# Kernel optimization log

Hardware: AMD Instinct MI355X
Metric: run time of the kernel (lower is better)

Reference implementation:

```python
import jax, jax.numpy as jnp
from jax import lax
import numpy as np

H = 256   # hidden size (hard-coded in module)
V = 10    # output classes


def setup_inputs() -> dict:
    key = jax.random.key(0)
    ks = jax.random.split(key, 7)
    B, T = 2048, 256
    x = jax.random.normal(ks[0], (B, T, 1), dtype=jnp.float32)
    # Linear weights stored as (in, out); torch nn.Linear computes x @ W.T + b,
    # equivalent here to x @ W_inout + b.
    s1 = 1.0  # fan_in of embed is 1
    sH = 1.0 / np.sqrt(H)
    W_e = jax.random.uniform(ks[1], (1, H), jnp.float32, -s1, s1)
    b_e = jax.random.uniform(ks[2], (H,), jnp.float32, -s1, s1)
    W_h = jax.random.uniform(ks[3], (H, H), jnp.float32, -sH, sH)
    b_h = jax.random.uniform(ks[4], (H,), jnp.float32, -sH, sH)
    W_o = jax.random.uniform(ks[5], (H, V), jnp.float32, -sH, sH)
    b_o = jax.random.uniform(ks[6], (V,), jnp.float32, -sH, sH)
    return {"x": x, "W_e": W_e, "b_e": b_e, "W_h": W_h, "b_h": b_h,
            "W_o": W_o, "b_o": b_o}


def reference(x, W_e, b_e, W_h, b_h, W_o, b_o):
    B, T, _ = x.shape
    # Embedding of each timestep is independent of h -> precompute in one batched op.
    inp_all = jnp.tanh(x @ W_e + b_e)            # [B, T, H]
    inp_tbh = jnp.swapaxes(inp_all, 0, 1)        # [T, B, H] for scan

    def step(h, inp_t):
        h = jnp.tanh((inp_t + h) @ W_h + b_h)    # [B, H]
        return h, None

    h0 = jnp.zeros((B, H), dtype=x.dtype)
    h_final, _ = lax.scan(step, h0, inp_tbh)
    return h_final @ W_o + b_o                   # [B, V]
```

## Files before the change

kernel.cpp:

```cpp
#include <hip/hip_runtime.h>

#define HDIM 256
#define TDIM 256
#define VOUT 10
#define BC   8

typedef _Float16 f16x8 __attribute__((ext_vector_type(8)));
typedef float    f32x4 __attribute__((ext_vector_type(4)));

__device__ __forceinline__ float fast_tanh(float a) {
    float e = __expf(2.0f * a);
    return 1.0f - 2.0f * __builtin_amdgcn_rcpf(e + 1.0f);
}

__device__ __forceinline__ unsigned pkrtz_u32(float a, float b) {
    auto v = __builtin_amdgcn_cvt_pkrtz(a, b);
    union { decltype(v) h; unsigned u; } cvt;
    cvt.h = v;
    return cvt.u;
}

__global__ __launch_bounds__(512, 1) void rnn_fwd_v13(
    const float* __restrict__ x,
    const float* __restrict__ We,
    const float* __restrict__ be,
    const float* __restrict__ Wh,
    const float* __restrict__ bh,
    const float* __restrict__ Wo,
    const float* __restrict__ bo,
    float* __restrict__ out)
{
    __shared__ __align__(16) char vraw[2][BC * HDIM * 2];
    __shared__ float x_lds[BC][TDIM + 2];
    __shared__ float h_fin[BC][HDIM + 1];

    const int tid = threadIdx.x;
    const int l   = tid & 63;
    const int w   = tid >> 6;
    const int n   = l & 15;
    const int rn  = n & 7;
    const int hi  = n >> 3;
    const int g   = l >> 4;
    const int r0  = blockIdx.x * BC;

    for (int k = tid; k < BC * TDIM; k += 512) {
        int r = k >> 8, t = k & 255;
        x_lds[r][t] = x[(r0 + r) * TDIM + t];
    }

    f16x8 wfrag[2][8];
    #pragma unroll
    for (int mt = 0; mt < 2; ++mt) {
        const int col = 32 * w + 16 * mt + n;
        #pragma unroll
        for (int kt = 0; kt < 8; ++kt) {
            #pragma unroll
            for (int e = 0; e < 8; ++e)
                wfrag[mt][kt][e] = (_Float16)Wh[(kt * 32 + g * 8 + e) * HDIM + col];
        }
    }

    f32x4 bh0, bh1;
    #pragma unroll
    for (int rg = 0; rg < 4; ++rg) {
        bh0[rg] = bh[32 * w + 4 * g + rg];
        bh1[rg] = bh[32 * w + 16 + 4 * g + rg];
    }

    float WeO[2][2], beO[2][2];
    #pragma unroll
    for (int mt = 0; mt < 2; ++mt) {
        const int hc = 32 * w + 16 * mt + 4 * g + 2 * hi;
        WeO[mt][0] = We[hc];     beO[mt][0] = be[hc];
        WeO[mt][1] = We[hc + 1]; beO[mt][1] = be[hc + 1];
    }

    const int base_r = g * 128 + rn * 16;
    int addr_w[2];
    #pragma unroll
    for (int mt = 0; mt < 2; ++mt)
        addr_w[mt] = (4 * w + 2 * mt + (g >> 1)) * 128 + rn * 16 + (g & 1) * 8 + hi * 4;

    __syncthreads();

    {
        const float xv = x_lds[rn][0];
        #pragma unroll
        for (int mt = 0; mt < 2; ++mt) {
            const float s0 = fast_tanh(xv * WeO[mt][0] + beO[mt][0]);
            const float s1 = fast_tanh(xv * WeO[mt][1] + beO[mt][1]);
            *(unsigned*)(&vraw[0][0] + addr_w[mt]) = pkrtz_u32(s0, s1);
        }
    }
    __syncthreads();

    int cur = 0;
    #pragma unroll 1
    for (int t = 0; t < TDIM - 1; ++t) {
        const char* vr = &vraw[cur][0];
        char*       vw = &vraw[cur ^ 1][0];

        const float xv = x_lds[rn][t + 1];
        f16x8 bfrag[8];
        #pragma unroll
        for (int kt = 0; kt < 8; ++kt)
            bfrag[kt] = *(const f16x8*)(vr + base_r + kt * 512);

        const f32x4 zero = {0.f, 0.f, 0.f, 0.f};
        f32x4 accE0 = __builtin_amdgcn_mfma_f32_16x16x32_f16(wfrag[0][0], bfrag[0], bh0,  0, 0, 0);
        f32x4 accE1 = __builtin_amdgcn_mfma_f32_16x16x32_f16(wfrag[1][0], bfrag[0], bh1,  0, 0, 0);
        f32x4 accO0 = __builtin_amdgcn_mfma_f32_16x16x32_f16(wfrag[0][1], bfrag[1], zero, 0, 0, 0);
        f32x4 accO1 = __builtin_amdgcn_mfma_f32_16x16x32_f16(wfrag[1][1], bfrag[1], zero, 0, 0, 0);
        #pragma unroll
        for (int kp = 1; kp < 4; ++kp) {
            accE0 = __builtin_amdgcn_mfma_f32_16x16x32_f16(wfrag[0][2 * kp],     bfrag[2 * kp],     accE0, 0, 0, 0);
            accE1 = __builtin_amdgcn_mfma_f32_16x16x32_f16(wfrag[1][2 * kp],     bfrag[2 * kp],     accE1, 0, 0, 0);
            accO0 = __builtin_amdgcn_mfma_f32_16x16x32_f16(wfrag[0][2 * kp + 1], bfrag[2 * kp + 1], accO0, 0, 0, 0);
            accO1 = __builtin_amdgcn_mfma_f32_16x16x32_f16(wfrag[1][2 * kp + 1], bfrag[2 * kp + 1], accO1, 0, 0, 0);
        }

        __builtin_amdgcn_sched_barrier(0);

        float ipp[2][2];
        #pragma unroll
        for (int mt = 0; mt < 2; ++mt) {
            ipp[mt][0] = 1.0f + fast_tanh(xv * WeO[mt][0] + beO[mt][0]);
            ipp[mt][1] = 1.0f + fast_tanh(xv * WeO[mt][1] + beO[mt][1]);
        }

        {
            const float a0 = (hi ? accE0[2] : accE0[0]) + (hi ? accO0[2] : accO0[0]);
            const float a1 = (hi ? accE0[3] : accE0[1]) + (hi ? accO0[3] : accO0[1]);
            const float r0v = __builtin_amdgcn_rcpf(__expf(2.0f * a0) + 1.0f);
            const float r1v = __builtin_amdgcn_rcpf(__expf(2.0f * a1) + 1.0f);
            const float s0 = fmaf(-2.0f, r0v, ipp[0][0]);
            const float s1 = fmaf(-2.0f, r1v, ipp[0][1]);
            *(unsigned*)(vw + addr_w[0]) = pkrtz_u32(s0, s1);
        }
        {
            const float a0 = (hi ? accE1[2] : accE1[0]) + (hi ? accO1[2] : accO1[0]);
            const float a1 = (hi ? accE1[3] : accE1[1]) + (hi ? accO1[3] : accO1[1]);
            const float r0v = __builtin_amdgcn_rcpf(__expf(2.0f * a0) + 1.0f);
            const float r1v = __builtin_amdgcn_rcpf(__expf(2.0f * a1) + 1.0f);
            const float s0 = fmaf(-2.0f, r0v, ipp[1][0]);
            const float s1 = fmaf(-2.0f, r1v, ipp[1][1]);
            *(unsigned*)(vw + addr_w[1]) = pkrtz_u32(s0, s1);
        }
        cur ^= 1;
        __syncthreads();
    }

    {
        const char* vr = &vraw[cur][0];
        f16x8 bfrag[8];
        #pragma unroll
        for (int kt = 0; kt < 8; ++kt)
            bfrag[kt] = *(const f16x8*)(vr + base_r + kt * 512);

        const f32x4 zero = {0.f, 0.f, 0.f, 0.f};
        f32x4 accE0 = __builtin_amdgcn_mfma_f32_16x16x32_f16(wfrag[0][0], bfrag[0], bh0,  0, 0, 0);
        f32x4 accE1 = __builtin_amdgcn_mfma_f32_16x16x32_f16(wfrag[1][0], bfrag[0], bh1,  0, 0, 0);
        f32x4 accO0 = __builtin_amdgcn_mfma_f32_16x16x32_f16(wfrag[0][1], bfrag[1], zero, 0, 0, 0);
        f32x4 accO1 = __builtin_amdgcn_mfma_f32_16x16x32_f16(wfrag[1][1], bfrag[1], zero, 0, 0, 0);
        #pragma unroll
        for (int kp = 1; kp < 4; ++kp) {
            accE0 = __builtin_amdgcn_mfma_f32_16x16x32_f16(wfrag[0][2 * kp],     bfrag[2 * kp],     accE0, 0, 0, 0);
            accE1 = __builtin_amdgcn_mfma_f32_16x16x32_f16(wfrag[1][2 * kp],     bfrag[2 * kp],     accE1, 0, 0, 0);
            accO0 = __builtin_amdgcn_mfma_f32_16x16x32_f16(wfrag[0][2 * kp + 1], bfrag[2 * kp + 1], accO0, 0, 0, 0);
            accO1 = __builtin_amdgcn_mfma_f32_16x16x32_f16(wfrag[1][2 * kp + 1], bfrag[2 * kp + 1], accO1, 0, 0, 0);
        }
        {
            const float a0 = (hi ? accE0[2] : accE0[0]) + (hi ? accO0[2] : accO0[0]);
            const float a1 = (hi ? accE0[3] : accE0[1]) + (hi ? accO0[3] : accO0[1]);
            const int hc = 32 * w + 4 * g + 2 * hi;
            h_fin[rn][hc + 0] = fast_tanh(a0);
            h_fin[rn][hc + 1] = fast_tanh(a1);
        }
        {
            const float a0 = (hi ? accE1[2] : accE1[0]) + (hi ? accO1[2] : accO1[0]);
            const float a1 = (hi ? accE1[3] : accE1[1]) + (hi ? accO1[3] : accO1[1]);
            const int hc = 32 * w + 16 + 4 * g + 2 * hi;
            h_fin[rn][hc + 0] = fast_tanh(a0);
            h_fin[rn][hc + 1] = fast_tanh(a1);
        }
    }
    __syncthreads();

    if (tid < BC * VOUT) {
        const int r = tid / VOUT, vc = tid - r * VOUT;
        float sacc = bo[vc];
        #pragma unroll 8
        for (int i = 0; i < HDIM; ++i)
            sacc = fmaf(h_fin[r][i], Wo[i * VOUT + vc], sacc);
        out[(r0 + r) * VOUT + vc] = sacc;
    }
}

extern "C" void kernel_launch(void* const* d_in, const int* in_sizes, int n_in,
                              void* d_out, int out_size, void* d_ws, size_t ws_size,
                              hipStream_t stream) {
    const float* x  = (const float*)d_in[0];
    const float* We = (const float*)d_in[1];
    const float* be = (const float*)d_in[2];
    const float* Wh = (const float*)d_in[3];
    const float* bh = (const float*)d_in[4];
    const float* Wo = (const float*)d_in[5];
    const float* bo = (const float*)d_in[6];
    float* out = (float*)d_out;

    const int B = in_sizes[0] / TDIM;
    const int nblocks = B / BC;

    rnn_fwd_v13<<<nblocks, 512, 0, stream>>>(x, We, be, Wh, bh, Wo, bo, out);
}
```

Before: 161.1 us.

## Prescale weights by two, remap lane output columns, hoist input tanh before MFMAs

New measurement: 149.9 us. -6.9%, faster.

```diff
diff --git a/kernel.cpp b/kernel.cpp
--- a/kernel.cpp
+++ b/kernel.cpp
@@ -8,8 +8,8 @@
 typedef _Float16 f16x8 __attribute__((ext_vector_type(8)));
 typedef float    f32x4 __attribute__((ext_vector_type(4)));
 
-__device__ __forceinline__ float fast_tanh(float a) {
-    float e = __expf(2.0f * a);
+__device__ __forceinline__ float tanh_2a(float u) {
+    float e = __expf(u);
     return 1.0f - 2.0f * __builtin_amdgcn_rcpf(e + 1.0f);
 }
 
@@ -20,7 +20,7 @@
     return cvt.u;
 }
 
-__global__ __launch_bounds__(512, 1) void rnn_fwd_v13(
+__global__ __launch_bounds__(512, 1) void rnn_fwd_v16(
     const float* __restrict__ x,
     const float* __restrict__ We,
     const float* __restrict__ be,
@@ -56,46 +56,45 @@
         for (int kt = 0; kt < 8; ++kt) {
             #pragma unroll
             for (int e = 0; e < 8; ++e)
-                wfrag[mt][kt][e] = (_Float16)Wh[(kt * 32 + g * 8 + e) * HDIM + col];
+                wfrag[mt][kt][e] = (_Float16)(2.0f * Wh[(kt * 32 + g * 8 + e) * HDIM + col]);
         }
     }
 
     f32x4 bh0, bh1;
     #pragma unroll
     for (int rg = 0; rg < 4; ++rg) {
-        bh0[rg] = bh[32 * w + 4 * g + rg];
-        bh1[rg] = bh[32 * w + 16 + 4 * g + rg];
-    }
-
-    float WeO[2][2], beO[2][2];
+        bh0[rg] = 2.0f * bh[32 * w + 4 * g + rg];
+        bh1[rg] = 2.0f * bh[32 * w + 16 + 4 * g + rg];
+    }
+
+    const int hc0 = 32 * w + 16 * hi + 4 * g;
+    float WeX[4], beX[4];
     #pragma unroll
-    for (int mt = 0; mt < 2; ++mt) {
-        const int hc = 32 * w + 16 * mt + 4 * g + 2 * hi;
-        WeO[mt][0] = We[hc];     beO[mt][0] = be[hc];
-        WeO[mt][1] = We[hc + 1]; beO[mt][1] = be[hc + 1];
+    for (int j = 0; j < 4; ++j) {
+        WeX[j] = 2.0f * We[hc0 + j];
+        beX[j] = 2.0f * be[hc0 + j];
     }
 
     const int base_r = g * 128 + rn * 16;
-    int addr_w[2];
-    #pragma unroll
-    for (int mt = 0; mt < 2; ++mt)
-        addr_w[mt] = (4 * w + 2 * mt + (g >> 1)) * 128 + rn * 16 + (g & 1) * 8 + hi * 4;
+    const int addr_w = (4 * w + 2 * hi + (g >> 1)) * 128 + rn * 16 + (g & 1) * 8;
 
     __syncthreads();
 
     {
         const float xv = x_lds[rn][0];
-        #pragma unroll
-        for (int mt = 0; mt < 2; ++mt) {
-            const float s0 = fast_tanh(xv * WeO[mt][0] + beO[mt][0]);
-            const float s1 = fast_tanh(xv * WeO[mt][1] + beO[mt][1]);
-            *(unsigned*)(&vraw[0][0] + addr_w[mt]) = pkrtz_u32(s0, s1);
-        }
+        float s[4];
+        #pragma unroll
+        for (int j = 0; j < 4; ++j)
+            s[j] = tanh_2a(fmaf(xv, WeX[j], beX[j]));
+        uint2 pk;
+        pk.x = pkrtz_u32(s[0], s[1]);
+        pk.y = pkrtz_u32(s[2], s[3]);
+        *(uint2*)(&vraw[0][0] + addr_w) = pk;
     }
     __syncthreads();
 
     int cur = 0;
-    #pragma unroll 1
+    #pragma unroll 2
     for (int t = 0; t < TDIM - 1; ++t) {
         const char* vr = &vraw[cur][0];
         char*       vw = &vraw[cur ^ 1][0];
@@ -105,6 +104,15 @@
         #pragma unroll
         for (int kt = 0; kt < 8; ++kt)
             bfrag[kt] = *(const f16x8*)(vr + base_r + kt * 512);
+
+        float ipp[4];
+        #pragma unroll
+        for (int j = 0; j < 4; ++j) {
+            const float u = fmaf(xv, WeX[j], beX[j]);
+            const float e = __expf(u);
+            const float r = __builtin_amdgcn_rcpf(e + 1.0f);
+            ipp[j] = fmaf(-2.0f, r, 2.0f);
+        }
 
         const f32x4 zero = {0.f, 0.f, 0.f, 0.f};
         f32x4 accE0 = __builtin_amdgcn_mfma_f32_16x16x32_f16(wfrag[0][0], bfrag[0], bh0,  0, 0, 0);
@@ -119,32 +127,19 @@
             accO1 = __builtin_amdgcn_mfma_f32_16x16x32_f16(wfrag[1][2 * kp + 1], bfrag[2 * kp + 1], accO1, 0, 0, 0);
         }
 
-        __builtin_amdgcn_sched_barrier(0);
-
-        float ipp[2][2];
-        #pragma unroll
-        for (int mt = 0; mt < 2; ++mt) {
-            ipp[mt][0] = 1.0f + fast_tanh(xv * WeO[mt][0] + beO[mt][0]);
-            ipp[mt][1] = 1.0f + fast_tanh(xv * WeO[mt][1] + beO[mt][1]);
-        }
-
         {
-            const float a0 = (hi ? accE0[2] : accE0[0]) + (hi ? accO0[2] : accO0[0]);
-            const float a1 = (hi ? accE0[3] : accE0[1]) + (hi ? accO0[3] : accO0[1]);
-            const float r0v = __builtin_amdgcn_rcpf(__expf(2.0f * a0) + 1.0f);
-            const float r1v = __builtin_amdgcn_rcpf(__expf(2.0f * a1) + 1.0f);
-            const float s0 = fmaf(-2.0f, r0v, ipp[0][0]);
-            const float s1 = fmaf(-2.0f, r1v, ipp[0][1]);
-            *(unsigned*)(vw + addr_w[0]) = pkrtz_u32(s0, s1);
-        }
-        {
-            const float a0 = (hi ? accE1[2] : accE1[0]) + (hi ? accO1[2] : accO1[0]);
-            const float a1 = (hi ? accE1[3] : accE1[1]) + (hi ? accO1[3] : accO1[1]);
-            const float r0v = __builtin_amdgcn_rcpf(__expf(2.0f * a0) + 1.0f);
-            const float r1v = __builtin_amdgcn_rcpf(__expf(2.0f * a1) + 1.0f);
-            const float s0 = fmaf(-2.0f, r0v, ipp[1][0]);
-            const float s1 = fmaf(-2.0f, r1v, ipp[1][1]);
-            *(unsigned*)(vw + addr_w[1]) = pkrtz_u32(s0, s1);
+            float sj[4];
+            #pragma unroll
+            for (int j = 0; j < 4; ++j) {
+                const float a = (hi ? accE1[j] : accE0[j]) + (hi ? accO1[j] : accO0[j]);
+                const float e = __expf(a);
+                const float r = __builtin_amdgcn_rcpf(e + 1.0f);
+                sj[j] = fmaf(-2.0f, r, ipp[j]);
+            }
+            uint2 pk;
+            pk.x = pkrtz_u32(sj[0], sj[1]);
+            pk.y = pkrtz_u32(sj[2], sj[3]);
+            *(uint2*)(vw + addr_w) = pk;
         }
         cur ^= 1;
         __syncthreads();
@@ -169,19 +164,10 @@
             accO0 = __builtin_amdgcn_mfma_f32_16x16x32_f16(wfrag[0][2 * kp + 1], bfrag[2 * kp + 1], accO0, 0, 0, 0);
             accO1 = __builtin_amdgcn_mfma_f32_16x16x32_f16(wfrag[1][2 * kp + 1], bfrag[2 * kp + 1], accO1, 0, 0, 0);
         }
-        {
-            const float a0 = (hi ? accE0[2] : accE0[0]) + (hi ? accO0[2] : accO0[0]);
-            const float a1 = (hi ? accE0[3] : accE0[1]) + (hi ? accO0[3] : accO0[1]);
-            const int hc = 32 * w + 4 * g + 2 * hi;
-            h_fin[rn][hc + 0] = fast_tanh(a0);
-            h_fin[rn][hc + 1] = fast_tanh(a1);
-        }
-        {
-            const float a0 = (hi ? accE1[2] : accE1[0]) + (hi ? accO1[2] : accO1[0]);
-            const float a1 = (hi ? accE1[3] : accE1[1]) + (hi ? accO1[3] : accO1[1]);
-            const int hc = 32 * w + 16 + 4 * g + 2 * hi;
-            h_fin[rn][hc + 0] = fast_tanh(a0);
-            h_fin[rn][hc + 1] = fast_tanh(a1);
+        #pragma unroll
+        for (int j = 0; j < 4; ++j) {
+            const float a = (hi ? accE1[j] : accE0[j]) + (hi ? accO1[j] : accO0[j]);
+            h_fin[rn][hc0 + j] = tanh_2a(a);
         }
     }
     __syncthreads();
@@ -211,5 +197,5 @@
     const int B = in_sizes[0] / TDIM;
     const int nblocks = B / BC;
 
-    rnn_fwd_v13<<<nblocks, 512, 0, stream>>>(x, We, be, Wh, bh, Wo, bo, out);
-}
+    rnn_fwd_v16<<<nblocks, 512, 0, stream>>>(x, We, be, Wh, bh, Wo, bo, out);
+}
```
